# Kernel tuning notes

Hardware: AMD Instinct MI355X
Metric: run time of the kernel (lower is better)

Reference implementation:

```python
import jax, jax.numpy as jnp
from jax import lax
import numpy as np


def _bilinear_up_kernel(ch, k):
    # replicates fill_up_weights for ConvTranspose2d weight [ch, 1, k, k]
    f = int(np.ceil(k / 2))
    c = (2 * f - 1 - f % 2) / (2.0 * f)
    i = np.arange(k)
    w1 = 1.0 - np.abs(i / f - c)
    w2 = np.outer(w1, w1).astype(np.float32)
    return jnp.asarray(np.tile(w2[None, None], (ch, 1, 1, 1)))


def _conv3x3(x, w, b):
    y = lax.conv_general_dilated(x, w, (1, 1), ((1, 1), (1, 1)),
                                 dimension_numbers=('NCHW', 'OIHW', 'NCHW'))
    return y + b[None, :, None, None]


def _dcn_bn_relu(x, w_om, b_om, w, b, gamma, beta, mean, var):
    # Modulated deformable conv v2 (3x3, pad 1, 1 deformable group) + BN(eval) + ReLU
    B, C, H, W = x.shape
    O = w.shape[0]
    om = _conv3x3(x, w_om, b_om)                      # [B,27,H,W]
    o1, o2, m = jnp.split(om, 3, axis=1)              # y-off, x-off, mask [B,9,H,W]
    m = jax.nn.sigmoid(m)
    kg = jnp.arange(3, dtype=x.dtype) - 1.0
    ky = jnp.repeat(kg, 3)                            # [9] row offsets (k = ky*3+kx)
    kx = jnp.tile(kg, 3)
    py = o1 + jnp.arange(H, dtype=x.dtype)[None, None, :, None] + ky[None, :, None, None]
    px = o2 + jnp.arange(W, dtype=x.dtype)[None, None, None, :] + kx[None, :, None, None]
    xh = jnp.transpose(x, (0, 2, 3, 1))               # [B,H,W,C]

    def samp(img, py_, px_):                          # img [H,W,C]; py_/px_ [9,H,W]
        y0 = jnp.floor(py_)
        x0 = jnp.floor(px_)
        wy = py_ - y0
        wx = px_ - x0
        y0i = y0.astype(jnp.int32)
        x0i = x0.astype(jnp.int32)

        def g(yi, xi):
            valid = ((yi >= 0) & (yi < H) & (xi >= 0) & (xi < W)).astype(img.dtype)
            v = img[jnp.clip(yi, 0, H - 1), jnp.clip(xi, 0, W - 1)]  # [9,H,W,C]
            return v * valid[..., None]

        return (g(y0i, x0i) * ((1 - wy) * (1 - wx))[..., None]
                + g(y0i, x0i + 1) * ((1 - wy) * wx)[..., None]
                + g(y0i + 1, x0i) * (wy * (1 - wx))[..., None]
                + g(y0i + 1, x0i + 1) * (wy * wx)[..., None])

    sampled = jax.vmap(samp)(xh, py, px)              # [B,9,H,W,C]
    sampled = sampled * m[..., None]
    wk = jnp.transpose(w.reshape(O, C, 9), (0, 2, 1))  # [O,9,C]
    y = jnp.einsum('bkhwc,okc->bohw', sampled, wk) + b[None, :, None, None]
    inv = gamma / jnp.sqrt(var + 1e-5)
    y = (y - mean[None, :, None, None]) * inv[None, :, None, None] + beta[None, :, None, None]
    return jax.nn.relu(y)


def _up(x, up_w, f):
    # depthwise ConvTranspose2d(k=2f, stride=f, pad=f//2, groups=C) as lhs-dilated conv
    k = 2 * f
    pad = k - 1 - (f // 2)
    wf = up_w[:, :, ::-1, ::-1]
    return lax.conv_general_dilated(x, wf, (1, 1), ((pad, pad), (pad, pad)),
                                    lhs_dilation=(f, f),
                                    dimension_numbers=('NCHW', 'OIHW', 'NCHW'),
                                    feature_group_count=x.shape[1])


def setup_inputs() -> dict:
    key = jax.random.key(0)
    ks = jax.random.split(key, 18)
    B, C, O, H, W, f = 2, 256, 128, 64, 128, 2
    H2, W2 = H * f, W * f
    n = jax.random.normal
    inp = {}
    inp['x'] = n(ks[0], (B, C, H, W), jnp.float32)
    inp['pre_x'] = n(ks[1], (B, O, H2, W2), jnp.float32)
    inp['proj_w_om'] = n(ks[2], (27, C, 3, 3), jnp.float32) * 0.01
    inp['proj_b_om'] = n(ks[3], (27,), jnp.float32) * 0.1
    inp['proj_w'] = n(ks[4], (O, C, 3, 3), jnp.float32) / np.sqrt(9 * C)
    inp['proj_b'] = n(ks[5], (O,), jnp.float32) * 0.01
    inp['proj_gamma'] = 1.0 + 0.1 * n(ks[6], (O,), jnp.float32)
    inp['proj_beta'] = 0.1 * n(ks[7], (O,), jnp.float32)
    inp['proj_mean'] = 0.1 * n(ks[8], (O,), jnp.float32)
    inp['proj_var'] = jax.random.uniform(ks[9], (O,), jnp.float32, 0.5, 1.5)
    inp['node_w_om'] = n(ks[10], (27, O, 3, 3), jnp.float32) * 0.01
    inp['node_b_om'] = n(ks[11], (27,), jnp.float32) * 0.1
    inp['node_w'] = n(ks[12], (O, O, 3, 3), jnp.float32) / np.sqrt(9 * O)
    inp['node_b'] = n(ks[13], (O,), jnp.float32) * 0.01
    inp['node_gamma'] = 1.0 + 0.1 * n(ks[14], (O,), jnp.float32)
    inp['node_beta'] = 0.1 * n(ks[15], (O,), jnp.float32)
    inp['node_mean'] = 0.1 * n(ks[16], (O,), jnp.float32)
    inp['node_var'] = jax.random.uniform(ks[17], (O,), jnp.float32, 0.5, 1.5)
    inp['up_w'] = _bilinear_up_kernel(O, 2 * f)
    return inp


def reference(x, pre_x, proj_w_om, proj_b_om, proj_w, proj_b, proj_gamma, proj_beta,
              proj_mean, proj_var, node_w_om, node_b_om, node_w, node_b, node_gamma,
              node_beta, node_mean, node_var, up_w):
    h = _dcn_bn_relu(x, proj_w_om, proj_b_om, proj_w, proj_b,
                     proj_gamma, proj_beta, proj_mean, proj_var)
    h = _up(h, up_w, 2)
    h = _dcn_bn_relu(h + pre_x, node_w_om, node_b_om, node_w, node_b,
                     node_gamma, node_beta, node_mean, node_var)
    return h
```

## Files before the change

### kernel.cpp

```cpp
#include <hip/hip_runtime.h>
#include <hip/hip_bf16.h>
#include <math.h>

typedef __bf16 bf16x8 __attribute__((ext_vector_type(8)));
typedef float  f32x4  __attribute__((ext_vector_type(4)));

static constexpr int BN2 = 2;
static constexpr int CA = 256, HA = 64, WA = 128;
static constexpr int OO = 128;
static constexpr int HC = 128, WC = 256, CC = 128;

__global__ void pack_w_kernel(const float* __restrict__ w, __bf16* __restrict__ out,
                              int Cin, int OT, int Oreal) {
    int NCH = Cin / 32;
    int idx = blockIdx.x * blockDim.x + threadIdx.x;
    int total = 9 * NCH * OT * 512;
    if (idx >= total) return;
    int j    = idx & 7;
    int lane = (idx >> 3) & 63;
    int ot   = (idx >> 9) % OT;
    int rest = (idx >> 9) / OT;
    int ch = rest % NCH;
    int k  = rest / NCH;
    int o = ot * 16 + (lane & 15);
    int c = ch * 32 + (lane >> 4) * 8 + j;
    float v = (o < Oreal) ? w[((size_t)o * Cin + c) * 9 + k] : 0.f;
    out[idx] = (__bf16)v;
}

template<int C, int HW>
__global__ __launch_bounds__(256) void to_cl_kernel(const float* __restrict__ x,
                                                    __bf16* __restrict__ xcl) {
    constexpr int NCB = C / 32;
    constexpr int NPB = HW / 64;
    int blk = blockIdx.x;
    int pblk = blk % NPB;
    int cblk = (blk / NPB) % NCB;
    int b = blk / (NPB * NCB);
    int t = threadIdx.x;
    __shared__ float st[32][65];
    int r = t >> 6, q = t & 63;
#pragma unroll
    for (int i = 0; i < 8; i++) {
        int c = cblk * 32 + i * 4 + r;
        st[i * 4 + r][q] = x[((size_t)b * C + c) * HW + pblk * 64 + q];
    }
    __syncthreads();
    int p = t >> 2, cq = t & 3;
    bf16x8 v;
#pragma unroll
    for (int j = 0; j < 8; j++) v[j] = (__bf16)st[cq * 8 + j][p];
    *reinterpret_cast<bf16x8*>(xcl + ((size_t)b * HW + pblk * 64 + p) * C + cblk * 32 + cq * 8) = v;
}

__global__ void bn_prepack_kernel(const float* __restrict__ g,  const float* __restrict__ be,
                                  const float* __restrict__ mu, const float* __restrict__ va,
                                  const float* __restrict__ bi,
                                  float* __restrict__ sc, float* __restrict__ sh) {
    int i = blockIdx.x * blockDim.x + threadIdx.x;
    if (i >= OO) return;
    float s = g[i] * rsqrtf(va[i] + 1e-5f);
    sc[i] = s;
    sh[i] = (bi[i] - mu[i]) * s + be[i];
}

__global__ void pack_upw_kernel(const float* __restrict__ upw, float* __restrict__ upwt) {
    int idx = blockIdx.x * blockDim.x + threadIdx.x;
    if (idx >= 16 * OO) return;
    int i = idx >> 7;
    int o = idx & 127;
    upwt[i * OO + o] = upw[o * 16 + i];
}

template<int C, int H, int W>
__global__ __launch_bounds__(256) void om_mfma_kernel(
    const __bf16* __restrict__ xcl,
    const __bf16* __restrict__ womp,
    const float* __restrict__ bom,
    float* __restrict__ omcl)
{
    constexpr int NCH = C / 32;
    constexpr int WS = 198;
    const int nwt = W / 64;
    int wt = blockIdx.x % nwt;
    int h  = (blockIdx.x / nwt) % H;
    int b  = blockIdx.x / (nwt * H);
    int t = threadIdx.x;
    int wave = t >> 6, lane = t & 63;
    int row = lane & 15, kg = lane >> 4;

    __shared__ __bf16 win[32 * WS];

    f32x4 acc0 = {0.f, 0.f, 0.f, 0.f};
    f32x4 acc1 = {0.f, 0.f, 0.f, 0.f};
    const __bf16* xb = xcl + (size_t)b * H * W * C;

    for (int ch = 0; ch < NCH; ch++) {
        for (int i = 0; i < 4; i++) {
            int idx = i * 256 + t;
            if (idx < 792) {
                int cq  = idx & 3;
                int pix = idx >> 2;
                int ry = pix / 66, rx = pix % 66;
                int y = h + ry - 1, xx = wt * 64 + rx - 1;
                bool valid = (y >= 0) && (y < H) && (xx >= 0) && (xx < W);
                int yc = min(max(y, 0), H - 1), xc = min(max(xx, 0), W - 1);
                uint4 u = *reinterpret_cast<const uint4*>(
                    xb + ((size_t)yc * W + xc) * C + ch * 32 + cq * 8);
                if (!valid) { u.x = 0; u.y = 0; u.z = 0; u.w = 0; }
                bf16x8 v = __builtin_bit_cast(bf16x8, u);
#pragma unroll
                for (int j = 0; j < 8; j++)
                    win[(cq * 8 + j) * WS + pix] = v[j];
            }
        }
        __syncthreads();
#pragma unroll
        for (int k = 0; k < 9; k++) {
            int off = (k / 3) * 66 + (k % 3) + wave * 16 + row;
            bf16x8 a;
#pragma unroll
            for (int j = 0; j < 8; j++)
                a[j] = win[(kg * 8 + j) * WS + off];
            const __bf16* wbc = womp + ((size_t)k * NCH + ch) * 1024 + lane * 8;
            bf16x8 b0 = *reinterpret_cast<const bf16x8*>(wbc);
            bf16x8 b1 = *reinterpret_cast<const bf16x8*>(wbc + 512);
            acc0 = __builtin_amdgcn_mfma_f32_16x16x32_bf16(a, b0, acc0, 0, 0, 0);
            acc1 = __builtin_amdgcn_mfma_f32_16x16x32_bf16(a, b1, acc1, 0, 0, 0);
        }
        __syncthreads();
    }

    float* ob = omcl + (((size_t)b * H + h) * W + wt * 64 + wave * 16 + kg * 4) * 32;
    float bb0 = bom[row];
#pragma unroll
    for (int j = 0; j < 4; j++)
        ob[(size_t)j * 32 + row] = acc0[j] + bb0;
    if (row < 11) {
        float bb1 = bom[16 + row];
#pragma unroll
        for (int j = 0; j < 4; j++)
            ob[(size_t)j * 32 + 16 + row] = acc1[j] + bb1;
    }
}

template<int C, int H, int W, int KS, bool CF_OUT>
__global__ __launch_bounds__(64 * KS) void dcn_mfma6_kernel(
    const __bf16* __restrict__ xcl,
    const float* __restrict__ omcl,
    const __bf16* __restrict__ wkp,
    const float* __restrict__ sc, const float* __restrict__ sh,
    float* __restrict__ outcf,
    __bf16* __restrict__ outcl)
{
    constexpr int NCH = C / 32;
    constexpr int CHW = NCH / KS;
    constexpr int NSW = 9 * CHW;
    static_assert(NSW % 2 == 0, "unroll-by-2 needs even NSW");
    constexpr int MAIN = 4608 + KS * 2560;
    constexpr int RED  = (KS - 1) * 9216;
    constexpr int SMEM = MAIN > RED ? MAIN : RED;

    const int nwt = W / 16;
    int wt = blockIdx.x % nwt;
    int h  = (blockIdx.x / nwt) % H;
    int b  = blockIdx.x / (nwt * H);
    int t = threadIdx.x;
    int wave = t >> 6, lane = t & 63;
    int row = lane & 15, kg = lane >> 4;
    int pos16 = lane >> 2, cq = lane & 3;

    __shared__ __align__(16) char smem[SMEM];
    int4*   pki  = reinterpret_cast<int4*>(smem);
    float4* pkw  = reinterpret_cast<float4*>(smem + 2304);
    __bf16* sbuf = reinterpret_cast<__bf16*>(smem + 4608);

    const float* omb = omcl + (((size_t)b * H + h) * W + wt * 16) * 32;
    for (int idx = t; idx < 144; idx += 64 * KS) {
        int p = idx & 15;
        int k = idx >> 4;
        float o1 = omb[p * 32 + k];
        float o2 = omb[p * 32 + 9 + k];
        float mm = omb[p * 32 + 18 + k];
        mm = 1.f / (1.f + expf(-mm));
        float py = o1 + (float)(h + k / 3 - 1);
        float px = o2 + (float)(wt * 16 + p + k % 3 - 1);
        float y0f = floorf(py), x0f = floorf(px);
        float wy = py - y0f, wx = px - x0f;
        int y0 = (int)y0f, x0 = (int)x0f;
        bool y0v = (y0 >= 0) && (y0 < H);
        bool y1v = (y0 + 1 >= 0) && (y0 + 1 < H);
        bool x0v = (x0 >= 0) && (x0 < W);
        bool x1v = (x0 + 1 >= 0) && (x0 + 1 < W);
        int y0c = min(max(y0, 0), H - 1) * W;
        int y1c = min(max(y0 + 1, 0), H - 1) * W;
        int x0c = min(max(x0, 0), W - 1);
        int x1c = min(max(x0 + 1, 0), W - 1);
        int4 pi;
        pi.x = (y0c + x0c) * C; pi.y = (y0c + x1c) * C;
        pi.z = (y1c + x0c) * C; pi.w = (y1c + x1c) * C;
        float4 pw;
        pw.x = (y0v && x0v) ? (1.f - wy) * (1.f - wx) * mm : 0.f;
        pw.y = (y0v && x1v) ? (1.f - wy) * wx * mm : 0.f;
        pw.z = (y1v && x0v) ? wy * (1.f - wx) * mm : 0.f;
        pw.w = (y1v && x1v) ? wy * wx * mm : 0.f;
        pki[idx] = pi;
        pkw[idx] = pw;
    }
    __syncthreads();

    f32x4 acc[8];
#pragma unroll
    for (int i = 0; i < 8; i++) acc[i] = {0.f, 0.f, 0.f, 0.f};

    const __bf16* xb = xcl + (size_t)b * H * W * C;
    __bf16* sb = sbuf + wave * 1280;
    __bf16* wp0 = sb + pos16 * 40 + cq * 8;
    const __bf16* rp0 = sb + row * 40 + kg * 8;

    uint4 u00, u01, u10, u11;
    float4 pwc;
    bf16x8 Ba[8], Bb[8];

    auto LOADG = [&](int ls) {
        int k = ls / CHW, chl = ls - k * CHW;
        int4 pi = pki[k * 16 + pos16];
        pwc = pkw[k * 16 + pos16];
        int cb = (wave * CHW + chl) * 32 + cq * 8;
        u00 = *reinterpret_cast<const uint4*>(xb + pi.x + cb);
        u01 = *reinterpret_cast<const uint4*>(xb + pi.y + cb);
        u10 = *reinterpret_cast<const uint4*>(xb + pi.z + cb);
        u11 = *reinterpret_cast<const uint4*>(xb + pi.w + cb);
    };
    auto LOADBA = [&](int ls) {
        int k = ls / CHW, chl = ls - k * CHW;
        int sg = k * NCH + wave * CHW + chl;
        const __bf16* wbc = wkp + (size_t)sg * 4096 + lane * 8;
#pragma unroll
        for (int ot = 0; ot < 8; ot++)
            Ba[ot] = *reinterpret_cast<const bf16x8*>(wbc + ot * 512);
    };
    auto LOADBB = [&](int ls) {
        int k = ls / CHW, chl = ls - k * CHW;
        int sg = k * NCH + wave * CHW + chl;
        const __bf16* wbc = wkp + (size_t)sg * 4096 + lane * 8;
#pragma unroll
        for (int ot = 0; ot < 8; ot++)
            Bb[ot] = *reinterpret_cast<const bf16x8*>(wbc + ot * 512);
    };
    auto BLEND = [&](int bufoff) {
        bf16x8 v00 = __builtin_bit_cast(bf16x8, u00);
        bf16x8 v01 = __builtin_bit_cast(bf16x8, u01);
        bf16x8 v10 = __builtin_bit_cast(bf16x8, u10);
        bf16x8 v11 = __builtin_bit_cast(bf16x8, u11);
        bf16x8 rg;
#pragma unroll
        for (int j = 0; j < 8; j++) {
            float sv = pwc.x * (float)v00[j] + pwc.y * (float)v01[j]
                     + pwc.z * (float)v10[j] + pwc.w * (float)v11[j];
            rg[j] = (__bf16)sv;
        }
        *reinterpret_cast<bf16x8*>(wp0 + bufoff) = rg;
    };
    auto MFMAA = [&](int bufoff) {
        bf16x8 a = *reinterpret_cast<const bf16x8*>(rp0 + bufoff);
#pragma unroll
        for (int ot = 0; ot < 8; ot++)
            acc[ot] = __builtin_amdgcn_mfma_f32_16x16x32_bf16(a, Ba[ot], acc[ot], 0, 0, 0);
    };
    auto MFMAB = [&](int bufoff) {
        bf16x8 a = *reinterpret_cast<const bf16x8*>(rp0 + bufoff);
#pragma unroll
        for (int ot = 0; ot < 8; ot++)
            acc[ot] = __builtin_amdgcn_mfma_f32_16x16x32_bf16(a, Bb[ot], acc[ot], 0, 0, 0);
    };

    LOADBA(0);
    LOADG(0);
    for (int s = 0; s < NSW; s += 2) {
        BLEND(0);
        LOADBB(s + 1);
        LOADG(s + 1);
        MFMAA(0);
        BLEND(640);
        if (s + 2 < NSW) { LOADBA(s + 2); LOADG(s + 2); }
        MFMAB(640);
    }

    __syncthreads();
    if (wave > 0) {
        float* rd = reinterpret_cast<float*>(smem) + (wave - 1) * 2304;
#pragma unroll
        for (int ot = 0; ot < 8; ot++)
            *reinterpret_cast<f32x4*>(rd + lane * 36 + ot * 4) = acc[ot];
    }
    __syncthreads();
    if (wave == 0) {
        for (int s = 0; s < KS - 1; s++) {
            float* rd = reinterpret_cast<float*>(smem) + s * 2304;
#pragma unroll
            for (int ot = 0; ot < 8; ot++) {
                f32x4 v = *reinterpret_cast<const f32x4*>(rd + lane * 36 + ot * 4);
                acc[ot] += v;
            }
        }
        if (CF_OUT) {
            float* ob = outcf + (size_t)b * OO * H * W + (size_t)h * W + wt * 16;
#pragma unroll
            for (int ot = 0; ot < 8; ot++) {
                int o = ot * 16 + row;
                float s = sc[o], hh = sh[o];
#pragma unroll
                for (int j = 0; j < 4; j++) {
                    float y = fmaxf(acc[ot][j] * s + hh, 0.f);
                    ob[(size_t)o * H * W + kg * 4 + j] = y;
                }
            }
        } else {
            __bf16* ob = outcl + (((size_t)b * H + h) * W + wt * 16) * OO;
#pragma unroll
            for (int ot = 0; ot < 8; ot++) {
                int o = ot * 16 + row;
                float s = sc[o], hh = sh[o];
#pragma unroll
                for (int j = 0; j < 4; j++) {
                    float y = fmaxf(acc[ot][j] * s + hh, 0.f);
                    ob[(size_t)(kg * 4 + j) * OO + o] = (__bf16)y;
                }
            }
        }
    }
}

__global__ __launch_bounds__(256) void upsample_cl_kernel(
    const __bf16* __restrict__ h1cl,
    const float* __restrict__ prex,
    const float* __restrict__ upwt,
    __bf16* __restrict__ zcl)
{
    int idx = blockIdx.x * blockDim.x + threadIdx.x;
    int x  = idx & (WC - 1);
    int y  = (idx >> 8) & (HC - 1);
    int cg = (idx >> 15) & 15;
    int b  = idx >> 19;

    int sy0, iy0, sy1, iy1, sx0, ix0, sx1, ix1;
    if (y & 1) { sy0 = (y - 1) >> 1; iy0 = 2; sy1 = sy0 + 1; iy1 = 0; }
    else       { sy0 = (y >> 1) - 1; iy0 = 3; sy1 = sy0 + 1; iy1 = 1; }
    if (x & 1) { sx0 = (x - 1) >> 1; ix0 = 2; sx1 = sx0 + 1; ix1 = 0; }
    else       { sx0 = (x >> 1) - 1; ix0 = 3; sx1 = sx0 + 1; ix1 = 1; }

    int c0 = cg * 8;
    float acc[8];
    const float* pp = prex + ((size_t)b * OO + c0) * (HC * WC) + (size_t)y * WC + x;
#pragma unroll
    for (int j = 0; j < 8; j++) acc[j] = pp[(size_t)j * HC * WC];

    bool y0v = sy0 >= 0, y1v = sy1 < HA;
    bool x0v = sx0 >= 0, x1v = sx1 < WA;
    const __bf16* hb = h1cl + (size_t)b * HA * WA * OO + c0;

    auto tap = [&](int sy, int sx, int wi) {
        uint4 u = *reinterpret_cast<const uint4*>(hb + ((size_t)sy * WA + sx) * OO);
        bf16x8 v = __builtin_bit_cast(bf16x8, u);
        const float* wp = upwt + wi * OO + c0;
#pragma unroll
        for (int j = 0; j < 8; j++) acc[j] += (float)v[j] * wp[j];
    };
    if (y0v && x0v) tap(sy0, sx0, iy0 * 4 + ix0);
    if (y0v && x1v) tap(sy0, sx1, iy0 * 4 + ix1);
    if (y1v && x0v) tap(sy1, sx0, iy1 * 4 + ix0);
    if (y1v && x1v) tap(sy1, sx1, iy1 * 4 + ix1);

    bf16x8 r;
#pragma unroll
    for (int j = 0; j < 8; j++) r[j] = (__bf16)acc[j];
    *reinterpret_cast<bf16x8*>(zcl + (((size_t)b * HC + y) * WC + x) * OO + c0) = r;
}

extern "C" void kernel_launch(void* const* d_in, const int* in_sizes, int n_in,
                              void* d_out, int out_size, void* d_ws, size_t ws_size,
                              hipStream_t stream) {
    (void)in_sizes; (void)n_in; (void)out_size; (void)ws_size;
    const float* x      = (const float*)d_in[0];
    const float* pre_x  = (const float*)d_in[1];
    const float* pwom   = (const float*)d_in[2];
    const float* pbom   = (const float*)d_in[3];
    const float* pw     = (const float*)d_in[4];
    const float* pb     = (const float*)d_in[5];
    const float* pgam   = (const float*)d_in[6];
    const float* pbet   = (const float*)d_in[7];
    const float* pmea   = (const float*)d_in[8];
    const float* pvar   = (const float*)d_in[9];
    const float* nwom   = (const float*)d_in[10];
    const float* nbom   = (const float*)d_in[11];
    const float* nw     = (const float*)d_in[12];
    const float* nb     = (const float*)d_in[13];
    const float* ngam   = (const float*)d_in[14];
    const float* nbet   = (const float*)d_in[15];
    const float* nmea   = (const float*)d_in[16];
    const float* nvar   = (const float*)d_in[17];
    const float* upw    = (const float*)d_in[18];
    float* out = (float*)d_out;

    char* wsb = (char*)d_ws;
    __bf16* xclA  = (__bf16*)(wsb + 0);
    __bf16* h1cl  = (__bf16*)(wsb + 8388608);
    __bf16* zcl   = (__bf16*)(wsb + 12582912);
    float*  omA   = (float*) (wsb + 29360128);
    float*  omC   = (float*) (wsb + 31457280);
    __bf16* wkAp  = (__bf16*)(wsb + 39845888);
    __bf16* wkCp  = (__bf16*)(wsb + 40435712);
    __bf16* womAp = (__bf16*)(wsb + 40730624);
    __bf16* womCp = (__bf16*)(wsb + 40878080);
    float*  upwt  = (float*) (wsb + 40951808);
    float*  scA   = (float*) (wsb + 40960000);
    float*  shA   = (float*) (wsb + 40960512);
    float*  scC   = (float*) (wsb + 40961024);
    float*  shC   = (float*) (wsb + 40961536);

    pack_w_kernel<<<1152, 256, 0, stream>>>(pw, wkAp, CA, 8, 128);
    pack_w_kernel<<<576, 256, 0, stream>>>(nw, wkCp, CC, 8, 128);
    pack_w_kernel<<<288, 256, 0, stream>>>(pwom, womAp, CA, 2, 27);
    pack_w_kernel<<<144, 256, 0, stream>>>(nwom, womCp, CC, 2, 27);
    bn_prepack_kernel<<<1, 128, 0, stream>>>(pgam, pbet, pmea, pvar, pb, scA, shA);
    bn_prepack_kernel<<<1, 128, 0, stream>>>(ngam, nbet, nmea, nvar, nb, scC, shC);
    pack_upw_kernel<<<8, 256, 0, stream>>>(upw, upwt);
    to_cl_kernel<CA, HA*WA><<<BN2 * (CA/32) * (HA*WA/64), 256, 0, stream>>>(x, xclA);

    om_mfma_kernel<CA, HA, WA><<<BN2 * HA * (WA/64), 256, 0, stream>>>(xclA, womAp, pbom, omA);
    dcn_mfma6_kernel<CA, HA, WA, 4, false><<<BN2 * HA * (WA/16), 256, 0, stream>>>(
        xclA, omA, wkAp, scA, shA, nullptr, h1cl);

    upsample_cl_kernel<<<(BN2 * 16 * HC * WC) / 256, 256, 0, stream>>>(h1cl, pre_x, upwt, zcl);

    om_mfma_kernel<CC, HC, WC><<<BN2 * HC * (WC/64), 256, 0, stream>>>(zcl, womCp, nbom, omC);
    dcn_mfma6_kernel<CC, HC, WC, 1, true><<<BN2 * HC * (WC/16), 64, 0, stream>>>(
        zcl, omC, wkCp, scC, shC, out, nullptr);
}
```

Before: 183.8 us.

## Gather MFMA A-operand directly in registers and deepen prefetch pipeline

The deformable conv kernel now has each lane gather and bilinearly blend the bf16 values that match its own MFMA A-operand position (row, kg). Before, values were blended into LDS and read back. This removes the per-step LDS write/read round trip and the shared staging buffer. The kernel also keeps two gather register sets and prefetches two steps ahead (A and B buffers). This adds register pressure and may lower occupancy or cause spills.

```diff
diff --git a/kernel.cpp b/kernel.cpp
--- a/kernel.cpp
+++ b/kernel.cpp
@@ -145,7 +145,7 @@
 }
 
 template<int C, int H, int W, int KS, bool CF_OUT>
-__global__ __launch_bounds__(64 * KS) void dcn_mfma6_kernel(
+__global__ __launch_bounds__(64 * KS) void dcn_mfma8_kernel(
     const __bf16* __restrict__ xcl,
     const float* __restrict__ omcl,
     const __bf16* __restrict__ wkp,
@@ -157,7 +157,7 @@
     constexpr int CHW = NCH / KS;
     constexpr int NSW = 9 * CHW;
     static_assert(NSW % 2 == 0, "unroll-by-2 needs even NSW");
-    constexpr int MAIN = 4608 + KS * 2560;
+    constexpr int MAIN = 4608;
     constexpr int RED  = (KS - 1) * 9216;
     constexpr int SMEM = MAIN > RED ? MAIN : RED;
 
@@ -168,12 +168,10 @@
     int t = threadIdx.x;
     int wave = t >> 6, lane = t & 63;
     int row = lane & 15, kg = lane >> 4;
-    int pos16 = lane >> 2, cq = lane & 3;
 
     __shared__ __align__(16) char smem[SMEM];
     int4*   pki  = reinterpret_cast<int4*>(smem);
     float4* pkw  = reinterpret_cast<float4*>(smem + 2304);
-    __bf16* sbuf = reinterpret_cast<__bf16*>(smem + 4608);
 
     const float* omb = omcl + (((size_t)b * H + h) * W + wt * 16) * 32;
     for (int idx = t; idx < 144; idx += 64 * KS) {
@@ -214,23 +212,30 @@
     for (int i = 0; i < 8; i++) acc[i] = {0.f, 0.f, 0.f, 0.f};
 
     const __bf16* xb = xcl + (size_t)b * H * W * C;
-    __bf16* sb = sbuf + wave * 1280;
-    __bf16* wp0 = sb + pos16 * 40 + cq * 8;
-    const __bf16* rp0 = sb + row * 40 + kg * 8;
-
-    uint4 u00, u01, u10, u11;
-    float4 pwc;
+
+    uint4 uA0, uA1, uA2, uA3, uB0, uB1, uB2, uB3;
+    float4 pwA, pwB;
     bf16x8 Ba[8], Bb[8];
 
-    auto LOADG = [&](int ls) {
+    auto LOADGA = [&](int ls) {
         int k = ls / CHW, chl = ls - k * CHW;
-        int4 pi = pki[k * 16 + pos16];
-        pwc = pkw[k * 16 + pos16];
-        int cb = (wave * CHW + chl) * 32 + cq * 8;
-        u00 = *reinterpret_cast<const uint4*>(xb + pi.x + cb);
-        u01 = *reinterpret_cast<const uint4*>(xb + pi.y + cb);
-        u10 = *reinterpret_cast<const uint4*>(xb + pi.z + cb);
-        u11 = *reinterpret_cast<const uint4*>(xb + pi.w + cb);
+        int4 pi = pki[k * 16 + row];
+        pwA = pkw[k * 16 + row];
+        int cb = (wave * CHW + chl) * 32 + kg * 8;
+        uA0 = *reinterpret_cast<const uint4*>(xb + pi.x + cb);
+        uA1 = *reinterpret_cast<const uint4*>(xb + pi.y + cb);
+        uA2 = *reinterpret_cast<const uint4*>(xb + pi.z + cb);
+        uA3 = *reinterpret_cast<const uint4*>(xb + pi.w + cb);
+    };
+    auto LOADGB = [&](int ls) {
+        int k = ls / CHW, chl = ls - k * CHW;
+        int4 pi = pki[k * 16 + row];
+        pwB = pkw[k * 16 + row];
+        int cb = (wave * CHW + chl) * 32 + kg * 8;
+        uB0 = *reinterpret_cast<const uint4*>(xb + pi.x + cb);
+        uB1 = *reinterpret_cast<const uint4*>(xb + pi.y + cb);
+        uB2 = *reinterpret_cast<const uint4*>(xb + pi.z + cb);
+        uB3 = *reinterpret_cast<const uint4*>(xb + pi.w + cb);
     };
     auto LOADBA = [&](int ls) {
         int k = ls / CHW, chl = ls - k * CHW;
@@ -248,11 +253,12 @@
         for (int ot = 0; ot < 8; ot++)
             Bb[ot] = *reinterpret_cast<const bf16x8*>(wbc + ot * 512);
     };
-    auto BLEND = [&](int bufoff) {
-        bf16x8 v00 = __builtin_bit_cast(bf16x8, u00);
-        bf16x8 v01 = __builtin_bit_cast(bf16x8, u01);
-        bf16x8 v10 = __builtin_bit_cast(bf16x8, u10);
-        bf16x8 v11 = __builtin_bit_cast(bf16x8, u11);
+    auto ABLEND = [&](const uint4& a0, const uint4& a1, const uint4& a2, const uint4& a3,
+                      const float4& pwc) -> bf16x8 {
+        bf16x8 v00 = __builtin_bit_cast(bf16x8, a0);
+        bf16x8 v01 = __builtin_bit_cast(bf16x8, a1);
+        bf16x8 v10 = __builtin_bit_cast(bf16x8, a2);
+        bf16x8 v11 = __builtin_bit_cast(bf16x8, a3);
         bf16x8 rg;
 #pragma unroll
         for (int j = 0; j < 8; j++) {
@@ -260,31 +266,26 @@
                      + pwc.z * (float)v10[j] + pwc.w * (float)v11[j];
             rg[j] = (__bf16)sv;
         }
-        *reinterpret_cast<bf16x8*>(wp0 + bufoff) = rg;
-    };
-    auto MFMAA = [&](int bufoff) {
-        bf16x8 a = *reinterpret_cast<const bf16x8*>(rp0 + bufoff);
-#pragma unroll
-        for (int ot = 0; ot < 8; ot++)
-            acc[ot] = __builtin_amdgcn_mfma_f32_16x16x32_bf16(a, Ba[ot], acc[ot], 0, 0, 0);
-    };
-    auto MFMAB = [&](int bufoff) {
-        bf16x8 a = *reinterpret_cast<const bf16x8*>(rp0 + bufoff);
-#pragma unroll
-        for (int ot = 0; ot < 8; ot++)
-            acc[ot] = __builtin_amdgcn_mfma_f32_16x16x32_bf16(a, Bb[ot], acc[ot], 0, 0, 0);
-    };
-
-    LOADBA(0);
-    LOADG(0);
+        return rg;
+    };
+
+    LOADBA(0); LOADGA(0);
+    LOADBB(1); LOADGB(1);
     for (int s = 0; s < NSW; s += 2) {
-        BLEND(0);
-        LOADBB(s + 1);
-        LOADG(s + 1);
-        MFMAA(0);
-        BLEND(640);
-        if (s + 2 < NSW) { LOADBA(s + 2); LOADG(s + 2); }
-        MFMAB(640);
+        {
+            bf16x8 a = ABLEND(uA0, uA1, uA2, uA3, pwA);
+#pragma unroll
+            for (int ot = 0; ot < 8; ot++)
+                acc[ot] = __builtin_amdgcn_mfma_f32_16x16x32_bf16(a, Ba[ot], acc[ot], 0, 0, 0);
+            if (s + 2 < NSW) { LOADBA(s + 2); LOADGA(s + 2); }
+        }
+        {
+            bf16x8 a = ABLEND(uB0, uB1, uB2, uB3, pwB);
+#pragma unroll
+            for (int ot = 0; ot < 8; ot++)
+                acc[ot] = __builtin_amdgcn_mfma_f32_16x16x32_bf16(a, Bb[ot], acc[ot], 0, 0, 0);
+            if (s + 3 < NSW) { LOADBB(s + 3); LOADGB(s + 3); }
+        }
     }
 
     __syncthreads();
@@ -429,12 +430,12 @@
     to_cl_kernel<CA, HA*WA><<<BN2 * (CA/32) * (HA*WA/64), 256, 0, stream>>>(x, xclA);
 
     om_mfma_kernel<CA, HA, WA><<<BN2 * HA * (WA/64), 256, 0, stream>>>(xclA, womAp, pbom, omA);
-    dcn_mfma6_kernel<CA, HA, WA, 4, false><<<BN2 * HA * (WA/16), 256, 0, stream>>>(
+    dcn_mfma8_kernel<CA, HA, WA, 4, false><<<BN2 * HA * (WA/16), 256, 0, stream>>>(
         xclA, omA, wkAp, scA, shA, nullptr, h1cl);
 
     upsample_cl_kernel<<<(BN2 * 16 * HC * WC) / 256, 256, 0, stream>>>(h1cl, pre_x, upwt, zcl);
 
     om_mfma_kernel<CC, HC, WC><<<BN2 * HC * (WC/64), 256, 0, stream>>>(zcl, womCp, nbom, omC);
-    dcn_mfma6_kernel<CC, HC, WC, 1, true><<<BN2 * HC * (WC/16), 64, 0, stream>>>(
+    dcn_mfma8_kernel<CC, HC, WC, 1, true><<<BN2 * HC * (WC/16), 64, 0, stream>>>(
         zcl, omC, wkCp, scC, shC, out, nullptr);
 }
```

Measured after the change: 239.2 us. 30.2% more time.

## Add software-pipelined DCN kernel with double-buffered weights for second stage

Applied to the files above, without the earlier changes.

Introduces a new deformable-conv MFMA kernel for the second (node) stage. Each 256-thread block runs four independent waves, and each wave handles one 16-pixel tile. Inside a wave, the 4-tap gather, bilinear blend and weight-fragment loads for the next step are issued before the MFMAs of the current step, using two register weight buffers and two LDS A-buffers. The aim is to hide gather and weight-load latency behind the matrix math and to use larger blocks than the earlier 64-thread launch. In exchange it roughly doubles the weight registers per wave, which may reduce occupancy.

```diff
diff --git a/kernel.cpp b/kernel.cpp
--- a/kernel.cpp
+++ b/kernel.cpp
@@ -332,6 +332,169 @@
     }
 }
 
+template<int C, int H, int W, bool CF_OUT>
+__global__ __launch_bounds__(256) void dcn_mfma9_kernel(
+    const __bf16* __restrict__ xcl,
+    const float* __restrict__ omcl,
+    const __bf16* __restrict__ wkp,
+    const float* __restrict__ sc, const float* __restrict__ sh,
+    float* __restrict__ outcf,
+    __bf16* __restrict__ outcl)
+{
+    constexpr int NCH = C / 32;
+    constexpr int NSW = 9 * NCH;
+    static_assert(NSW % 2 == 0, "unroll-by-2 needs even NSW");
+
+    int t = threadIdx.x;
+    int wave = t >> 6, lane = t & 63;
+    int row = lane & 15, kg = lane >> 4;
+    int pos16 = lane >> 2, cq = lane & 3;
+
+    __shared__ __align__(16) char smem[4 * 7168];
+    char* ws = smem + wave * 7168;
+    int4*   pki = reinterpret_cast<int4*>(ws);
+    float4* pkw = reinterpret_cast<float4*>(ws + 2304);
+    __bf16* sb  = reinterpret_cast<__bf16*>(ws + 4608);
+
+    const int nwt = W / 16;
+    int tile = blockIdx.x * 4 + wave;
+    int wt = tile % nwt;
+    int h  = (tile / nwt) % H;
+    int b  = tile / (nwt * H);
+
+    const float* omb = omcl + (((size_t)b * H + h) * W + wt * 16) * 32;
+    for (int idx = lane; idx < 144; idx += 64) {
+        int p = idx & 15;
+        int k = idx >> 4;
+        float o1 = omb[p * 32 + k];
+        float o2 = omb[p * 32 + 9 + k];
+        float mm = omb[p * 32 + 18 + k];
+        mm = 1.f / (1.f + expf(-mm));
+        float py = o1 + (float)(h + k / 3 - 1);
+        float px = o2 + (float)(wt * 16 + p + k % 3 - 1);
+        float y0f = floorf(py), x0f = floorf(px);
+        float wy = py - y0f, wx = px - x0f;
+        int y0 = (int)y0f, x0 = (int)x0f;
+        bool y0v = (y0 >= 0) && (y0 < H);
+        bool y1v = (y0 + 1 >= 0) && (y0 + 1 < H);
+        bool x0v = (x0 >= 0) && (x0 < W);
+        bool x1v = (x0 + 1 >= 0) && (x0 + 1 < W);
+        int y0c = min(max(y0, 0), H - 1) * W;
+        int y1c = min(max(y0 + 1, 0), H - 1) * W;
+        int x0c = min(max(x0, 0), W - 1);
+        int x1c = min(max(x0 + 1, 0), W - 1);
+        int4 pi;
+        pi.x = (y0c + x0c) * C; pi.y = (y0c + x1c) * C;
+        pi.z = (y1c + x0c) * C; pi.w = (y1c + x1c) * C;
+        float4 pw;
+        pw.x = (y0v && x0v) ? (1.f - wy) * (1.f - wx) * mm : 0.f;
+        pw.y = (y0v && x1v) ? (1.f - wy) * wx * mm : 0.f;
+        pw.z = (y1v && x0v) ? wy * (1.f - wx) * mm : 0.f;
+        pw.w = (y1v && x1v) ? wy * wx * mm : 0.f;
+        pki[idx] = pi;
+        pkw[idx] = pw;
+    }
+
+    f32x4 acc[8];
+#pragma unroll
+    for (int i = 0; i < 8; i++) acc[i] = {0.f, 0.f, 0.f, 0.f};
+
+    const __bf16* xb = xcl + (size_t)b * H * W * C;
+    __bf16* wp0 = sb + pos16 * 40 + cq * 8;
+    const __bf16* rp0 = sb + row * 40 + kg * 8;
+
+    uint4 u00, u01, u10, u11;
+    float4 pwc;
+    bf16x8 Ba[8], Bb[8];
+
+    auto LOADG = [&](int ls) {
+        int k = ls / NCH, chl = ls - k * NCH;
+        int4 pi = pki[k * 16 + pos16];
+        pwc = pkw[k * 16 + pos16];
+        int cb = chl * 32 + cq * 8;
+        u00 = *reinterpret_cast<const uint4*>(xb + pi.x + cb);
+        u01 = *reinterpret_cast<const uint4*>(xb + pi.y + cb);
+        u10 = *reinterpret_cast<const uint4*>(xb + pi.z + cb);
+        u11 = *reinterpret_cast<const uint4*>(xb + pi.w + cb);
+    };
+    auto LOADBA = [&](int ls) {
+        const __bf16* wbc = wkp + (size_t)ls * 4096 + lane * 8;
+#pragma unroll
+        for (int ot = 0; ot < 8; ot++)
+            Ba[ot] = *reinterpret_cast<const bf16x8*>(wbc + ot * 512);
+    };
+    auto LOADBB = [&](int ls) {
+        const __bf16* wbc = wkp + (size_t)ls * 4096 + lane * 8;
+#pragma unroll
+        for (int ot = 0; ot < 8; ot++)
+            Bb[ot] = *reinterpret_cast<const bf16x8*>(wbc + ot * 512);
+    };
+    auto BLEND = [&](int bufoff) {
+        bf16x8 v00 = __builtin_bit_cast(bf16x8, u00);
+        bf16x8 v01 = __builtin_bit_cast(bf16x8, u01);
+        bf16x8 v10 = __builtin_bit_cast(bf16x8, u10);
+        bf16x8 v11 = __builtin_bit_cast(bf16x8, u11);
+        bf16x8 rg;
+#pragma unroll
+        for (int j = 0; j < 8; j++) {
+            float sv = pwc.x * (float)v00[j] + pwc.y * (float)v01[j]
+                     + pwc.z * (float)v10[j] + pwc.w * (float)v11[j];
+            rg[j] = (__bf16)sv;
+        }
+        *reinterpret_cast<bf16x8*>(wp0 + bufoff) = rg;
+    };
+    auto MFMAA = [&](int bufoff) {
+        bf16x8 a = *reinterpret_cast<const bf16x8*>(rp0 + bufoff);
+#pragma unroll
+        for (int ot = 0; ot < 8; ot++)
+            acc[ot] = __builtin_amdgcn_mfma_f32_16x16x32_bf16(a, Ba[ot], acc[ot], 0, 0, 0);
+    };
+    auto MFMAB = [&](int bufoff) {
+        bf16x8 a = *reinterpret_cast<const bf16x8*>(rp0 + bufoff);
+#pragma unroll
+        for (int ot = 0; ot < 8; ot++)
+            acc[ot] = __builtin_amdgcn_mfma_f32_16x16x32_bf16(a, Bb[ot], acc[ot], 0, 0, 0);
+    };
+
+    LOADBA(0);
+    LOADG(0);
+    for (int s = 0; s < NSW; s += 2) {
+        BLEND(0);
+        LOADBB(s + 1);
+        LOADG(s + 1);
+        MFMAA(0);
+        BLEND(640);
+        if (s + 2 < NSW) { LOADBA(s + 2); LOADG(s + 2); }
+        MFMAB(640);
+    }
+
+    if (CF_OUT) {
+        float* ob = outcf + (size_t)b * OO * H * W + (size_t)h * W + wt * 16;
+#pragma unroll
+        for (int ot = 0; ot < 8; ot++) {
+            int o = ot * 16 + row;
+            float s = sc[o], hh = sh[o];
+#pragma unroll
+            for (int j = 0; j < 4; j++) {
+                float y = fmaxf(acc[ot][j] * s + hh, 0.f);
+                ob[(size_t)o * H * W + kg * 4 + j] = y;
+            }
+        }
+    } else {
+        __bf16* ob = outcl + (((size_t)b * H + h) * W + wt * 16) * OO;
+#pragma unroll
+        for (int ot = 0; ot < 8; ot++) {
+            int o = ot * 16 + row;
+            float s = sc[o], hh = sh[o];
+#pragma unroll
+            for (int j = 0; j < 4; j++) {
+                float y = fmaxf(acc[ot][j] * s + hh, 0.f);
+                ob[(size_t)(kg * 4 + j) * OO + o] = (__bf16)y;
+            }
+        }
+    }
+}
+
 __global__ __launch_bounds__(256) void upsample_cl_kernel(
     const __bf16* __restrict__ h1cl,
     const float* __restrict__ prex,
@@ -435,6 +598,6 @@
     upsample_cl_kernel<<<(BN2 * 16 * HC * WC) / 256, 256, 0, stream>>>(h1cl, pre_x, upwt, zcl);
 
     om_mfma_kernel<CC, HC, WC><<<BN2 * HC * (WC/64), 256, 0, stream>>>(zcl, womCp, nbom, omC);
-    dcn_mfma6_kernel<CC, HC, WC, 1, true><<<BN2 * HC * (WC/16), 64, 0, stream>>>(
+    dcn_mfma9_kernel<CC, HC, WC, true><<<BN2 * HC * (WC/16) / 4, 256, 0, stream>>>(
         zcl, omC, wkCp, scC, shC, out, nullptr);
 }
```

Result: no change. 184.7 us (+0.5%).
